# Kernel tuning notes

Measured on AMD Instinct MI355X. Metric: run time of the kernel, lower is better.

## Reference

```python
import jax, jax.numpy as jnp
import numpy as np

N_NODES = 50000
N_EDGES = 800000
N_GRAPHS = 128
HIDDEN = 64
HEADS = 2
OUT = 4
NEG_SLOPE = 0.2
ALPHA_FLAG = 0.05


def _gat_conv(x, src, dst, W, a_src, a_dst, b):
    # PyG GATConv, concat=False (mean over heads), self-loops already appended.
    N = x.shape[0]
    H, C = a_src.shape
    xh = (x @ W).reshape(N, H, C)                       # [N,H,C]
    s_src = (xh * a_src).sum(-1)                        # [N,H]
    s_dst = (xh * a_dst).sum(-1)                        # [N,H]
    e = s_src[src] + s_dst[dst]                         # [E,H]
    e = jnp.where(e > 0, e, NEG_SLOPE * e)              # LeakyReLU(0.2)
    emax = jax.ops.segment_max(e, dst, num_segments=N)  # per-dst softmax max
    emax = jnp.where(jnp.isfinite(emax), emax, 0.0)
    p = jnp.exp(e - emax[dst])
    denom = jax.ops.segment_sum(p, dst, num_segments=N)
    alpha = p / (denom[dst] + 1e-16)                    # [E,H]
    out = jax.ops.segment_sum(alpha[:, :, None] * xh[src], dst, num_segments=N)
    return out.mean(axis=1) + b                         # [N,HIDDEN]


def setup_inputs() -> dict:
    key = jax.random.key(0)
    ks = jax.random.split(key, 32)
    f = lambda k, shape, s=0.1: (jax.random.normal(k, shape) * s).astype(jnp.float32)
    inp = {}
    inp['x_all'] = jax.random.normal(ks[0], (N_NODES, 8), dtype=jnp.float32)
    inp['climber'] = jax.random.normal(ks[1], (N_GRAPHS, 4), dtype=jnp.float32)
    inp['edge_index'] = jax.random.randint(ks[2], (2, N_EDGES), 0, N_NODES)
    inp['batch'] = jnp.sort(jax.random.randint(ks[3], (N_NODES,), 0, N_GRAPHS))
    H = HIDDEN
    inp['W_in'] = f(ks[4], (6, H)); inp['b_in'] = jnp.zeros((H,), jnp.float32)
    inp['W_c'] = f(ks[5], (4, H)); inp['b_c'] = jnp.zeros((H,), jnp.float32)
    inp['W_f1'] = f(ks[6], (H, 2 * H)); inp['b_f1'] = jnp.zeros((2 * H,), jnp.float32)
    inp['W_f2'] = f(ks[7], (H, 2 * H)); inp['b_f2'] = jnp.zeros((2 * H,), jnp.float32)
    inp['W_g1'] = f(ks[8], (H, HEADS * H)); inp['a_src1'] = f(ks[9], (HEADS, H)); inp['a_dst1'] = f(ks[10], (HEADS, H)); inp['b_g1'] = jnp.zeros((H,), jnp.float32)
    inp['W_g2'] = f(ks[11], (H, HEADS * H)); inp['a_src2'] = f(ks[12], (HEADS, H)); inp['a_dst2'] = f(ks[13], (HEADS, H)); inp['b_g2'] = jnp.zeros((H,), jnp.float32)
    inp['W_cl1'] = f(ks[14], (H, H)); inp['b_cl1'] = jnp.zeros((H,), jnp.float32)
    inp['W_cl2'] = f(ks[15], (H, OUT)); inp['b_cl2'] = jnp.zeros((OUT,), jnp.float32)
    inp['W_fh1'] = f(ks[16], (2, 8), 0.001); inp['b_fh1'] = jnp.zeros((8,), jnp.float32)
    inp['W_fh2'] = f(ks[17], (8, OUT), 0.001); inp['b_fh2'] = jnp.zeros((OUT,), jnp.float32)
    return inp


def reference(x_all, climber, edge_index, batch, W_in, b_in, W_c, b_c,
              W_f1, b_f1, W_f2, b_f2,
              W_g1, a_src1, a_dst1, b_g1,
              W_g2, a_src2, a_dst2, b_g2,
              W_cl1, b_cl1, W_cl2, b_cl2,
              W_fh1, b_fh1, W_fh2, b_fh2):
    N = x_all.shape[0]
    flags = x_all[:, -2:]
    x = x_all[:, :-2]
    # climber embedding (eval mode -> dropout is identity)
    c = jax.nn.relu(climber @ W_c + b_c)                 # [G,H]
    x = x @ W_in + b_in                                  # [N,H]
    # FiLM 1
    gb = c @ W_f1 + b_f1
    gamma, beta = jnp.split(gb, 2, axis=-1)
    x = x * (1.0 + gamma[batch]) + beta[batch]
    # add self-loops (PyG GATConv default)
    loop = jnp.arange(N, dtype=edge_index.dtype)
    src = jnp.concatenate([edge_index[0], loop])
    dst = jnp.concatenate([edge_index[1], loop])
    x = jax.nn.relu(_gat_conv(x, src, dst, W_g1, a_src1, a_dst1, b_g1))
    # FiLM 2
    gb = c @ W_f2 + b_f2
    gamma, beta = jnp.split(gb, 2, axis=-1)
    x = x * (1.0 + gamma[batch]) + beta[batch]
    x = jax.nn.relu(_gat_conv(x, src, dst, W_g2, a_src2, a_dst2, b_g2))
    logits_main = jax.nn.relu(x @ W_cl1 + b_cl1) @ W_cl2 + b_cl2
    logits_flag = jax.nn.relu(flags @ W_fh1 + b_fh1) @ W_fh2 + b_fh2
    return logits_main + ALPHA_FLAG * logits_flag
```

## Files before the change

### kernel.cpp

```cpp
#include <hip/hip_runtime.h>
#include <hip/hip_fp16.h>

#define NEG_SLOPE 0.2f
#define ALPHA_FLAG 0.05f

static inline size_t align256(size_t x) { return (x + 255) & ~(size_t)255; }

__global__ void prep_kernel(const float* __restrict__ climber,
                            const float* __restrict__ W_c, const float* __restrict__ b_c,
                            const float* __restrict__ W_f1, const float* __restrict__ b_f1,
                            const float* __restrict__ W_f2, const float* __restrict__ b_f2,
                            float* __restrict__ gb1, float* __restrict__ gb2) {
    __shared__ float c_sh[64];
    int g = blockIdx.x, t = threadIdx.x;
    if (t < 64) {
        float acc = b_c[t];
#pragma unroll
        for (int k = 0; k < 4; ++k) acc = fmaf(climber[g * 4 + k], W_c[k * 64 + t], acc);
        c_sh[t] = fmaxf(acc, 0.f);
    }
    __syncthreads();
    float a1 = b_f1[t], a2 = b_f2[t];
#pragma unroll 8
    for (int h = 0; h < 64; ++h) {
        float cv = c_sh[h];
        a1 = fmaf(cv, W_f1[h * 128 + t], a1);
        a2 = fmaf(cv, W_f2[h * 128 + t], a2);
    }
    gb1[g * 128 + t] = a1;
    gb2[g * 128 + t] = a2;
}

__global__ void init_counts_kernel(int* __restrict__ counts, int N) {
    int i = blockIdx.x * blockDim.x + threadIdx.x;
    if (i < N) counts[i] = 1;
}

__global__ void hist_kernel(const int* __restrict__ dst, int E, int* __restrict__ counts) {
    int i = blockIdx.x * blockDim.x + threadIdx.x;
    if (i < E) atomicAdd(&counts[dst[i]], 1);
}

#define SCAN_CHUNK 1024
__global__ void scan_partial_kernel(const int* __restrict__ counts, int* __restrict__ block_sums, int N) {
    __shared__ int sh[256];
    int b = blockIdx.x, t = threadIdx.x;
    int idx0 = b * SCAN_CHUNK + t * 4;
    int s = 0;
    if (idx0 + 3 < N) {
        int4 v = *(const int4*)&counts[idx0];
        s = v.x + v.y + v.z + v.w;
    } else {
#pragma unroll
        for (int u = 0; u < 4; ++u) if (idx0 + u < N) s += counts[idx0 + u];
    }
    sh[t] = s;
    __syncthreads();
#pragma unroll
    for (int off = 128; off; off >>= 1) {
        if (t < off) sh[t] += sh[t + off];
        __syncthreads();
    }
    if (t == 0) block_sums[b] = sh[0];
}

__global__ void scan_blocksums_kernel(const int* __restrict__ block_sums, int* __restrict__ block_bases,
                                      int nb, int* __restrict__ row_ptr, int N) {
    __shared__ int sh[256];
    int t = threadIdx.x;
    int v = (t < nb) ? block_sums[t] : 0;
    sh[t] = v;
    __syncthreads();
#pragma unroll
    for (int off = 1; off < 256; off <<= 1) {
        int add = (t >= off) ? sh[t - off] : 0;
        __syncthreads();
        sh[t] += add;
        __syncthreads();
    }
    if (t < nb) block_bases[t] = sh[t] - v;
    if (t == nb - 1) row_ptr[N] = sh[t];
}

__global__ void scan_final_kernel(const int* __restrict__ counts, const int* __restrict__ block_bases,
                                  int* __restrict__ row_ptr, int* __restrict__ fill, int N) {
    __shared__ int sh[256];
    int b = blockIdx.x, t = threadIdx.x;
    int idx0 = b * SCAN_CHUNK + t * 4;
    int c[4];
    if (idx0 + 3 < N) {
        int4 v = *(const int4*)&counts[idx0];
        c[0] = v.x; c[1] = v.y; c[2] = v.z; c[3] = v.w;
    } else {
#pragma unroll
        for (int u = 0; u < 4; ++u) c[u] = (idx0 + u < N) ? counts[idx0 + u] : 0;
    }
    int s = c[0] + c[1] + c[2] + c[3];
    sh[t] = s;
    __syncthreads();
#pragma unroll
    for (int off = 1; off < 256; off <<= 1) {
        int add = (t >= off) ? sh[t - off] : 0;
        __syncthreads();
        sh[t] += add;
        __syncthreads();
    }
    int run = block_bases[b] + sh[t] - s;
#pragma unroll
    for (int u = 0; u < 4; ++u) {
        if (idx0 + u < N) {
            row_ptr[idx0 + u] = run;
            fill[idx0 + u] = run;
            run += c[u];
        }
    }
}

__global__ void scatter_kernel(const int* __restrict__ src, const int* __restrict__ dst,
                               int E, int N, int* __restrict__ fill, int* __restrict__ csr_src) {
    int i = blockIdx.x * blockDim.x + threadIdx.x;
    if (i >= E + N) return;
    int s, d;
    if (i < E) { s = src[i]; d = dst[i]; }
    else       { s = i - E; d = s; }
    int pos = atomicAdd(&fill[d], 1);
    csr_src[pos] = s;
}

#define XH_NB 32
__global__ __launch_bounds__(256, 4) void xh_kernel(
    const float* __restrict__ x, const float* __restrict__ W_g,
    const float* __restrict__ a_src, const float* __restrict__ a_dst,
    __half* __restrict__ xh, float* __restrict__ s_src, float* __restrict__ s_dst,
    int N, int in_mode,
    const float* __restrict__ x_all, const int* __restrict__ batch,
    const float* __restrict__ W_in, const float* __restrict__ b_in,
    const float* __restrict__ gb1) {
    __shared__ float x_sh[XH_NB * 64];
    __shared__ float win_sh[6 * 64 + 64];
    int t = threadIdx.x;
    int base = blockIdx.x * XH_NB;
    if (in_mode) {
        for (int i = t; i < 448; i += 256)
            win_sh[i] = (i < 384) ? W_in[i] : b_in[i - 384];
        __syncthreads();
        int nd = t >> 3;
        int jb = (t & 7) * 8;
        int n = base + nd;
        if (n < N) {
            float4 a = *(const float4*)&x_all[(size_t)n * 8];
            float2 b = *(const float2*)&x_all[(size_t)n * 8 + 4];
            float xa[6] = {a.x, a.y, a.z, a.w, b.x, b.y};
            int g = batch[n];
            const float* gbrow = &gb1[g * 128];
#pragma unroll
            for (int jj = 0; jj < 8; ++jj) {
                int j = jb + jj;
                float acc = win_sh[384 + j];
#pragma unroll
                for (int k = 0; k < 6; ++k) acc = fmaf(xa[k], win_sh[k * 64 + j], acc);
                x_sh[nd * 64 + j] = acc * (1.f + gbrow[j]) + gbrow[64 + j];
            }
        } else {
#pragma unroll
            for (int jj = 0; jj < 8; ++jj) x_sh[nd * 64 + jb + jj] = 0.f;
        }
    } else {
        int nvalid = N - base; if (nvalid > XH_NB) nvalid = XH_NB;
        int nfloats = nvalid * 64;
#pragma unroll
        for (int rep = 0; rep < 2; ++rep) {
            int i = t * 4 + rep * 1024;
            float4 v = (i < nfloats) ? *(const float4*)&x[(size_t)base * 64 + i]
                                     : make_float4(0.f, 0.f, 0.f, 0.f);
            *(float4*)&x_sh[i] = v;
        }
    }
    __syncthreads();
    int c = t & 63;
    int g = t >> 6;
    float acc0[8], acc1[8];
#pragma unroll
    for (int i = 0; i < 8; ++i) { acc0[i] = 0.f; acc1[i] = 0.f; }
    const float* W0 = W_g + c;
    const float* W1 = W_g + 64 + c;
#pragma unroll 2
    for (int k = 0; k < 64; k += 4) {
        float w0[4], w1[4];
#pragma unroll
        for (int u = 0; u < 4; ++u) { w0[u] = W0[(k + u) * 128]; w1[u] = W1[(k + u) * 128]; }
#pragma unroll
        for (int i = 0; i < 8; ++i) {
            float4 xv = *(const float4*)&x_sh[(g * 8 + i) * 64 + k];
            acc0[i] = fmaf(xv.x, w0[0], acc0[i]);
            acc0[i] = fmaf(xv.y, w0[1], acc0[i]);
            acc0[i] = fmaf(xv.z, w0[2], acc0[i]);
            acc0[i] = fmaf(xv.w, w0[3], acc0[i]);
            acc1[i] = fmaf(xv.x, w1[0], acc1[i]);
            acc1[i] = fmaf(xv.y, w1[1], acc1[i]);
            acc1[i] = fmaf(xv.z, w1[2], acc1[i]);
            acc1[i] = fmaf(xv.w, w1[3], acc1[i]);
        }
    }
    float as0 = a_src[c], ad0 = a_dst[c];
    float as1 = a_src[64 + c], ad1 = a_dst[64 + c];
#pragma unroll
    for (int i = 0; i < 8; ++i) {
        int n = base + g * 8 + i;
        float ps0 = acc0[i] * as0, pd0 = acc0[i] * ad0;
        float ps1 = acc1[i] * as1, pd1 = acc1[i] * ad1;
#pragma unroll
        for (int off = 32; off; off >>= 1) {
            ps0 += __shfl_xor(ps0, off); pd0 += __shfl_xor(pd0, off);
            ps1 += __shfl_xor(ps1, off); pd1 += __shfl_xor(pd1, off);
        }
        if (n < N) {
            if (c == 0) {
                s_src[n * 2 + 0] = ps0; s_src[n * 2 + 1] = ps1;
                s_dst[n * 2 + 0] = pd0; s_dst[n * 2 + 1] = pd1;
            }
            __half2 hv = __floats2half2_rn(acc0[i], acc1[i]);
            *(__half2*)&xh[(size_t)n * 128 + c * 2] = hv;
        }
    }
}

__global__ __launch_bounds__(256) void agg_kernel(
    const __half* __restrict__ xh, const float* __restrict__ s_src,
    const float* __restrict__ s_dst, const int* __restrict__ row_ptr,
    const int* __restrict__ csr_src, const float* __restrict__ b_g,
    const int* __restrict__ batch, const float* __restrict__ gb_film,
    float* __restrict__ xout, int N, int mode,
    const float* __restrict__ x_all,
    const float* __restrict__ W_cl1, const float* __restrict__ b_cl1,
    const float* __restrict__ W_cl2, const float* __restrict__ b_cl2,
    const float* __restrict__ W_fh1, const float* __restrict__ b_fh1,
    const float* __restrict__ W_fh2, const float* __restrict__ b_fh2,
    float* __restrict__ out) {
    __shared__ float4 ps_sh[4][64];
    __shared__ float vh_sh[4][128];
    int lane = threadIdx.x & 63;
    int w = threadIdx.x >> 6;
    int n = (blockIdx.x * blockDim.x + threadIdx.x) >> 6;
    if (n >= N) return;
    int beg = row_ptr[n], end = row_ptr[n + 1];
    float2 sd = *(const float2*)&s_dst[n * 2];
    const char* xhb = (const char*)xh;
    int sub = lane >> 4;
    unsigned q16 = (unsigned)(lane & 15) * 16u;
    float acc[8] = {0.f, 0.f, 0.f, 0.f, 0.f, 0.f, 0.f, 0.f};
    float dp0 = 0.f, dp1 = 0.f;
    for (int chunk = beg; chunk < end; chunk += 64) {
        int m = end - chunk; if (m > 64) m = 64;
        float p0 = 0.f, p1 = 0.f; unsigned sb = 0;
        if (lane < m) {
            int s = csr_src[chunk + lane];
            sb = (unsigned)s << 8;
            float2 ss = *(const float2*)&s_src[s * 2];
            float e0 = ss.x + sd.x;
            float e1 = ss.y + sd.y;
            e0 = (e0 > 0.f) ? e0 : NEG_SLOPE * e0;
            e1 = (e1 > 0.f) ? e1 : NEG_SLOPE * e1;
            p0 = __expf(e0); p1 = __expf(e1);
        }
        dp0 += p0; dp1 += p1;
        ps_sh[w][lane] = make_float4(p0, p1, __uint_as_float(sb), 0.f);
        int mr = (m + 3) & ~3;
        for (int j = 0; j < mr; j += 4) {
            float4 ps = ps_sh[w][j + sub];
            unsigned voff = __float_as_uint(ps.z) + q16;
            uint4 hv = *(const uint4*)(xhb + voff);
            float2 c0 = __half22float2(*(__half2*)&hv.x);
            float2 c1 = __half22float2(*(__half2*)&hv.y);
            float2 c2 = __half22float2(*(__half2*)&hv.z);
            float2 c3 = __half22float2(*(__half2*)&hv.w);
            acc[0] = fmaf(ps.x, c0.x, acc[0]); acc[1] = fmaf(ps.y, c0.y, acc[1]);
            acc[2] = fmaf(ps.x, c1.x, acc[2]); acc[3] = fmaf(ps.y, c1.y, acc[3]);
            acc[4] = fmaf(ps.x, c2.x, acc[4]); acc[5] = fmaf(ps.y, c2.y, acc[5]);
            acc[6] = fmaf(ps.x, c3.x, acc[6]); acc[7] = fmaf(ps.y, c3.y, acc[7]);
        }
    }
#pragma unroll
    for (int u = 0; u < 8; ++u) {
        acc[u] += __shfl_xor(acc[u], 16);
        acc[u] += __shfl_xor(acc[u], 32);
    }
#pragma unroll
    for (int off = 32; off; off >>= 1) {
        dp0 += __shfl_xor(dp0, off);
        dp1 += __shfl_xor(dp1, off);
    }
    if (lane < 16) {
        int q4 = lane * 4;
        vh_sh[w][q4 + 0] = acc[0]; vh_sh[w][q4 + 1] = acc[2];
        vh_sh[w][q4 + 2] = acc[4]; vh_sh[w][q4 + 3] = acc[6];
        vh_sh[w][64 + q4 + 0] = acc[1]; vh_sh[w][64 + q4 + 1] = acc[3];
        vh_sh[w][64 + q4 + 2] = acc[5]; vh_sh[w][64 + q4 + 3] = acc[7];
    }
    float A0 = vh_sh[w][lane];
    float A1 = vh_sh[w][64 + lane];
    float v = 0.5f * (A0 / (dp0 + 1e-16f) + A1 / (dp1 + 1e-16f)) + b_g[lane];
    v = fmaxf(v, 0.f);
    if (mode == 0) {
        int g = batch[n];
        v = v * (1.f + gb_film[g * 128 + lane]) + gb_film[g * 128 + 64 + lane];
        xout[(size_t)n * 64 + lane] = v;
        return;
    }
    vh_sh[w][lane] = v;
    float h = b_cl1[lane];
#pragma unroll 4
    for (int k = 0; k < 64; k += 4) {
        float4 vq = *(const float4*)&vh_sh[w][k];
        h = fmaf(vq.x, W_cl1[(k + 0) * 64 + lane], h);
        h = fmaf(vq.y, W_cl1[(k + 1) * 64 + lane], h);
        h = fmaf(vq.z, W_cl1[(k + 2) * 64 + lane], h);
        h = fmaf(vq.w, W_cl1[(k + 3) * 64 + lane], h);
    }
    h = fmaxf(h, 0.f);
    float4 w2 = *(const float4*)&W_cl2[lane * 4];
    float o0 = h * w2.x, o1 = h * w2.y, o2 = h * w2.z, o3 = h * w2.w;
#pragma unroll
    for (int off = 32; off; off >>= 1) {
        o0 += __shfl_xor(o0, off); o1 += __shfl_xor(o1, off);
        o2 += __shfl_xor(o2, off); o3 += __shfl_xor(o3, off);
    }
    if (lane < 4) {
        float f0 = x_all[(size_t)n * 8 + 6], f1 = x_all[(size_t)n * 8 + 7];
        float lf = b_fh2[lane];
#pragma unroll
        for (int m = 0; m < 8; ++m) {
            float fm = fmaxf(fmaf(f0, W_fh1[m], fmaf(f1, W_fh1[8 + m], b_fh1[m])), 0.f);
            lf = fmaf(fm, W_fh2[m * 4 + lane], lf);
        }
        float om = (lane == 0) ? o0 : (lane == 1) ? o1 : (lane == 2) ? o2 : o3;
        out[(size_t)n * 4 + lane] = om + b_cl2[lane] + ALPHA_FLAG * lf;
    }
}

extern "C" void kernel_launch(void* const* d_in, const int* in_sizes, int n_in,
                              void* d_out, int out_size, void* d_ws, size_t ws_size,
                              hipStream_t stream) {
    const float* x_all   = (const float*)d_in[0];
    const float* climber = (const float*)d_in[1];
    const int*   eidx    = (const int*)d_in[2];
    const int*   batch   = (const int*)d_in[3];
    const float* W_in  = (const float*)d_in[4];
    const float* b_in  = (const float*)d_in[5];
    const float* W_c   = (const float*)d_in[6];
    const float* b_c   = (const float*)d_in[7];
    const float* W_f1  = (const float*)d_in[8];
    const float* b_f1  = (const float*)d_in[9];
    const float* W_f2  = (const float*)d_in[10];
    const float* b_f2  = (const float*)d_in[11];
    const float* W_g1  = (const float*)d_in[12];
    const float* a_s1  = (const float*)d_in[13];
    const float* a_d1  = (const float*)d_in[14];
    const float* b_g1  = (const float*)d_in[15];
    const float* W_g2  = (const float*)d_in[16];
    const float* a_s2  = (const float*)d_in[17];
    const float* a_d2  = (const float*)d_in[18];
    const float* b_g2  = (const float*)d_in[19];
    const float* W_cl1 = (const float*)d_in[20];
    const float* b_cl1 = (const float*)d_in[21];
    const float* W_cl2 = (const float*)d_in[22];
    const float* b_cl2 = (const float*)d_in[23];
    const float* W_fh1 = (const float*)d_in[24];
    const float* b_fh1 = (const float*)d_in[25];
    const float* W_fh2 = (const float*)d_in[26];
    const float* b_fh2 = (const float*)d_in[27];
    float* out = (float*)d_out;

    const int N = in_sizes[0] / 8;
    const int E = in_sizes[2] / 2;
    const int G = in_sizes[1] / 4;
    const int* src = eidx;
    const int* dst = eidx + E;
    const int NB_SCAN = (N + SCAN_CHUNK - 1) / SCAN_CHUNK;

    char* ws = (char*)d_ws;
    size_t off = 0;
    auto alloc = [&](size_t bytes) { char* p = ws + off; off += align256(bytes); return p; };
    float*  gb1     = (float*)alloc((size_t)G * 128 * 4);
    float*  gb2     = (float*)alloc((size_t)G * 128 * 4);
    float*  xbuf    = (float*)alloc((size_t)N * 64 * 4);
    __half* xh      = (__half*)alloc((size_t)N * 128 * 2);
    float*  s_src   = (float*)alloc((size_t)N * 2 * 4);
    float*  s_dst   = (float*)alloc((size_t)N * 2 * 4);
    int*    counts  = (int*)alloc((size_t)N * 4);
    int*    fill    = (int*)alloc((size_t)N * 4);
    int*    row_ptr = (int*)alloc((size_t)(N + 1) * 4);
    int*    csr_src = (int*)alloc((size_t)(E + N) * 4);
    int*    bsums   = (int*)alloc((size_t)256 * 4);
    int*    bbases  = (int*)alloc((size_t)256 * 4);
    (void)ws_size;

    prep_kernel<<<G, 128, 0, stream>>>(climber, W_c, b_c, W_f1, b_f1, W_f2, b_f2, gb1, gb2);
    init_counts_kernel<<<(N + 255) / 256, 256, 0, stream>>>(counts, N);
    hist_kernel<<<(E + 255) / 256, 256, 0, stream>>>(dst, E, counts);
    scan_partial_kernel<<<NB_SCAN, 256, 0, stream>>>(counts, bsums, N);
    scan_blocksums_kernel<<<1, 256, 0, stream>>>(bsums, bbases, NB_SCAN, row_ptr, N);
    scan_final_kernel<<<NB_SCAN, 256, 0, stream>>>(counts, bbases, row_ptr, fill, N);
    scatter_kernel<<<(E + N + 255) / 256, 256, 0, stream>>>(src, dst, E, N, fill, csr_src);
    xh_kernel<<<(N + XH_NB - 1) / XH_NB, 256, 0, stream>>>(nullptr, W_g1, a_s1, a_d1, xh,
                                                           s_src, s_dst, N, 1,
                                                           x_all, batch, W_in, b_in, gb1);
    agg_kernel<<<(N * 64 + 255) / 256, 256, 0, stream>>>(xh, s_src, s_dst, row_ptr, csr_src,
                                                         b_g1, batch, gb2, xbuf, N, 0,
                                                         nullptr, nullptr, nullptr, nullptr,
                                                         nullptr, nullptr, nullptr, nullptr,
                                                         nullptr, nullptr);
    xh_kernel<<<(N + XH_NB - 1) / XH_NB, 256, 0, stream>>>(xbuf, W_g2, a_s2, a_d2, xh,
                                                           s_src, s_dst, N, 0,
                                                           nullptr, nullptr, nullptr, nullptr, nullptr);
    agg_kernel<<<(N * 64 + 255) / 256, 256, 0, stream>>>(xh, s_src, s_dst, row_ptr, csr_src,
                                                         b_g2, batch, nullptr, nullptr, N, 1,
                                                         x_all, W_cl1, b_cl1, W_cl2, b_cl2,
                                                         W_fh1, b_fh1, W_fh2, b_fh2, out);
}
```

Measured before the change: 266.8 us.

## Pre-normalize attention weights and use fp16 dot2 for head-mean aggregation

Result: no change. 266.0 us (-0.3%).

```diff
diff --git a/kernel.cpp b/kernel.cpp
--- a/kernel.cpp
+++ b/kernel.cpp
@@ -3,6 +3,12 @@
 
 #define NEG_SLOPE 0.2f
 #define ALPHA_FLAG 0.05f
+
+typedef _Float16 h2t __attribute__((ext_vector_type(2)));
+union h2u { unsigned u; h2t h; __half2 hh; float f; };
+static __device__ __forceinline__ h2t u_as_h2(unsigned u) { h2u c; c.u = u; return c.h; }
+static __device__ __forceinline__ float h2_as_f(__half2 h) { h2u c; c.hh = h; return c.f; }
+static __device__ __forceinline__ h2t f_as_h2(float f) { h2u c; c.f = f; return c.h; }
 
 static inline size_t align256(size_t x) { return (x + 255) & ~(size_t)255; }
 
@@ -225,6 +231,18 @@
     }
 }
 
+static __device__ __forceinline__ float dot2acc(unsigned xbits, h2t w, float acc) {
+#if __has_builtin(__builtin_amdgcn_fdot2)
+    return __builtin_amdgcn_fdot2(u_as_h2(xbits), w, acc, false);
+#else
+    h2u cx; cx.u = xbits;
+    float2 xf = __half22float2(cx.hh);
+    h2u cw; cw.h = w;
+    float2 wf = __half22float2(cw.hh);
+    return fmaf(xf.x, wf.x, fmaf(xf.y, wf.y, acc));
+#endif
+}
+
 __global__ __launch_bounds__(256) void agg_kernel(
     const __half* __restrict__ xh, const float* __restrict__ s_src,
     const float* __restrict__ s_dst, const int* __restrict__ row_ptr,
@@ -237,69 +255,104 @@
     const float* __restrict__ W_fh1, const float* __restrict__ b_fh1,
     const float* __restrict__ W_fh2, const float* __restrict__ b_fh2,
     float* __restrict__ out) {
-    __shared__ float4 ps_sh[4][64];
-    __shared__ float vh_sh[4][128];
+    __shared__ float2 ps_sh[4][64];
+    __shared__ float vh_sh[4][64];
     int lane = threadIdx.x & 63;
     int w = threadIdx.x >> 6;
     int n = (blockIdx.x * blockDim.x + threadIdx.x) >> 6;
     if (n >= N) return;
     int beg = row_ptr[n], end = row_ptr[n + 1];
+    int deg = end - beg;
     float2 sd = *(const float2*)&s_dst[n * 2];
     const char* xhb = (const char*)xh;
     int sub = lane >> 4;
     unsigned q16 = (unsigned)(lane & 15) * 16u;
-    float acc[8] = {0.f, 0.f, 0.f, 0.f, 0.f, 0.f, 0.f, 0.f};
-    float dp0 = 0.f, dp1 = 0.f;
-    for (int chunk = beg; chunk < end; chunk += 64) {
-        int m = end - chunk; if (m > 64) m = 64;
+    float acc[4] = {0.f, 0.f, 0.f, 0.f};
+
+    if (deg <= 64) {
         float p0 = 0.f, p1 = 0.f; unsigned sb = 0;
-        if (lane < m) {
-            int s = csr_src[chunk + lane];
+        if (lane < deg) {
+            int s = csr_src[beg + lane];
             sb = (unsigned)s << 8;
             float2 ss = *(const float2*)&s_src[s * 2];
-            float e0 = ss.x + sd.x;
-            float e1 = ss.y + sd.y;
+            float e0 = ss.x + sd.x, e1 = ss.y + sd.y;
             e0 = (e0 > 0.f) ? e0 : NEG_SLOPE * e0;
             e1 = (e1 > 0.f) ? e1 : NEG_SLOPE * e1;
             p0 = __expf(e0); p1 = __expf(e1);
         }
-        dp0 += p0; dp1 += p1;
-        ps_sh[w][lane] = make_float4(p0, p1, __uint_as_float(sb), 0.f);
-        int mr = (m + 3) & ~3;
+        float dp0 = p0, dp1 = p1;
+#pragma unroll
+        for (int off = 32; off; off >>= 1) {
+            dp0 += __shfl_xor(dp0, off);
+            dp1 += __shfl_xor(dp1, off);
+        }
+        float i0 = 0.5f / (dp0 + 1e-16f), i1 = 0.5f / (dp1 + 1e-16f);
+        ps_sh[w][lane] = make_float2(h2_as_f(__floats2half2_rn(p0 * i0, p1 * i1)),
+                                     __uint_as_float(sb));
+        int mr = (deg + 3) & ~3;
         for (int j = 0; j < mr; j += 4) {
-            float4 ps = ps_sh[w][j + sub];
-            unsigned voff = __float_as_uint(ps.z) + q16;
+            float2 ps = ps_sh[w][j + sub];
+            h2t wpk = f_as_h2(ps.x);
+            unsigned voff = __float_as_uint(ps.y) + q16;
             uint4 hv = *(const uint4*)(xhb + voff);
-            float2 c0 = __half22float2(*(__half2*)&hv.x);
-            float2 c1 = __half22float2(*(__half2*)&hv.y);
-            float2 c2 = __half22float2(*(__half2*)&hv.z);
-            float2 c3 = __half22float2(*(__half2*)&hv.w);
-            acc[0] = fmaf(ps.x, c0.x, acc[0]); acc[1] = fmaf(ps.y, c0.y, acc[1]);
-            acc[2] = fmaf(ps.x, c1.x, acc[2]); acc[3] = fmaf(ps.y, c1.y, acc[3]);
-            acc[4] = fmaf(ps.x, c2.x, acc[4]); acc[5] = fmaf(ps.y, c2.y, acc[5]);
-            acc[6] = fmaf(ps.x, c3.x, acc[6]); acc[7] = fmaf(ps.y, c3.y, acc[7]);
-        }
-    }
-#pragma unroll
-    for (int u = 0; u < 8; ++u) {
+            acc[0] = dot2acc(hv.x, wpk, acc[0]);
+            acc[1] = dot2acc(hv.y, wpk, acc[1]);
+            acc[2] = dot2acc(hv.z, wpk, acc[2]);
+            acc[3] = dot2acc(hv.w, wpk, acc[3]);
+        }
+    } else {
+        float dp0 = 0.f, dp1 = 0.f;
+        for (int chunk = beg; chunk < end; chunk += 64) {
+            int m = end - chunk; if (m > 64) m = 64;
+            if (lane < m) {
+                int s = csr_src[chunk + lane];
+                float2 ss = *(const float2*)&s_src[s * 2];
+                float e0 = ss.x + sd.x, e1 = ss.y + sd.y;
+                e0 = (e0 > 0.f) ? e0 : NEG_SLOPE * e0;
+                e1 = (e1 > 0.f) ? e1 : NEG_SLOPE * e1;
+                dp0 += __expf(e0); dp1 += __expf(e1);
+            }
+        }
+#pragma unroll
+        for (int off = 32; off; off >>= 1) {
+            dp0 += __shfl_xor(dp0, off);
+            dp1 += __shfl_xor(dp1, off);
+        }
+        float i0 = 0.5f / (dp0 + 1e-16f), i1 = 0.5f / (dp1 + 1e-16f);
+        for (int chunk = beg; chunk < end; chunk += 64) {
+            int m = end - chunk; if (m > 64) m = 64;
+            float p0 = 0.f, p1 = 0.f; unsigned sb = 0;
+            if (lane < m) {
+                int s = csr_src[chunk + lane];
+                sb = (unsigned)s << 8;
+                float2 ss = *(const float2*)&s_src[s * 2];
+                float e0 = ss.x + sd.x, e1 = ss.y + sd.y;
+                e0 = (e0 > 0.f) ? e0 : NEG_SLOPE * e0;
+                e1 = (e1 > 0.f) ? e1 : NEG_SLOPE * e1;
+                p0 = __expf(e0); p1 = __expf(e1);
+            }
+            ps_sh[w][lane] = make_float2(h2_as_f(__floats2half2_rn(p0 * i0, p1 * i1)),
+                                         __uint_as_float(sb));
+            int mr = (m + 3) & ~3;
+            for (int j = 0; j < mr; j += 4) {
+                float2 ps = ps_sh[w][j + sub];
+                h2t wpk = f_as_h2(ps.x);
+                unsigned voff = __float_as_uint(ps.y) + q16;
+                uint4 hv = *(const uint4*)(xhb + voff);
+                acc[0] = dot2acc(hv.x, wpk, acc[0]);
+                acc[1] = dot2acc(hv.y, wpk, acc[1]);
+                acc[2] = dot2acc(hv.z, wpk, acc[2]);
+                acc[3] = dot2acc(hv.w, wpk, acc[3]);
+            }
+        }
+    }
+#pragma unroll
+    for (int u = 0; u < 4; ++u) {
         acc[u] += __shfl_xor(acc[u], 16);
         acc[u] += __shfl_xor(acc[u], 32);
     }
-#pragma unroll
-    for (int off = 32; off; off >>= 1) {
-        dp0 += __shfl_xor(dp0, off);
-        dp1 += __shfl_xor(dp1, off);
-    }
-    if (lane < 16) {
-        int q4 = lane * 4;
-        vh_sh[w][q4 + 0] = acc[0]; vh_sh[w][q4 + 1] = acc[2];
-        vh_sh[w][q4 + 2] = acc[4]; vh_sh[w][q4 + 3] = acc[6];
-        vh_sh[w][64 + q4 + 0] = acc[1]; vh_sh[w][64 + q4 + 1] = acc[3];
-        vh_sh[w][64 + q4 + 2] = acc[5]; vh_sh[w][64 + q4 + 3] = acc[7];
-    }
-    float A0 = vh_sh[w][lane];
-    float A1 = vh_sh[w][64 + lane];
-    float v = 0.5f * (A0 / (dp0 + 1e-16f) + A1 / (dp1 + 1e-16f)) + b_g[lane];
+    if (lane < 16) *(float4*)&vh_sh[w][lane * 4] = make_float4(acc[0], acc[1], acc[2], acc[3]);
+    float v = vh_sh[w][lane] + b_g[lane];
     v = fmaxf(v, 0.f);
     if (mode == 0) {
         int g = batch[n];
```
